# Optimization experiments

Hardware: AMD Instinct MI355X
Metric: run time of the kernel (lower is better)

The kernel has to match this reference:

```python
import jax, jax.numpy as jnp
import numpy as np

P, Q, R = 3, 1, 0          # CliffordAlgebra(p=3, q=1, r=0)
N = P + Q + R
ALG = 1 << N               # 16 basis blades
SHIFTS = (1, 2, 4)


def _cayley():
    """Cayley table C[i,j,k]: blade_i * blade_j = C[i,j,i^j] * blade_{i^j}."""
    metric = [1.0] * P + [-1.0] * Q + [0.0] * R
    C = np.zeros((ALG, ALG, ALG), np.float32)
    for a in range(ALG):
        for b in range(ALG):
            x = a >> 1
            s = 0
            while x:                       # reordering sign
                s += bin(x & b).count('1')
                x >>= 1
            val = -1.0 if (s & 1) else 1.0
            for i in range(N):             # metric for repeated basis vectors
                if (a & b) >> i & 1:
                    val *= metric[i]
            C[a, b, a ^ b] = val
    return C

_C = _cayley()
C0 = jnp.asarray(_C[:, :, 0])                        # grade-0 slice: <a*b>_0
A = jnp.asarray((_C - _C.transpose(1, 0, 2)) / 2.0)  # antisym: (ab - ba)/2
VEC_MASK = jnp.asarray(np.array([1.0 if bin(i).count('1') == 1 else 0.0 for i in range(ALG)], np.float32))
BIV_MASK = jnp.asarray(np.array([1.0 if bin(i).count('1') == 2 else 0.0 for i in range(ALG)], np.float32))


def setup_inputs() -> dict:
    key = jax.random.key(0)
    k1, k2 = jax.random.split(key, 2)
    B, T, D = 8, 4096, 1024
    return {
        "x": jax.random.normal(k1, (B, T, D), jnp.float32),
        "gate_w": jax.random.normal(k2, (D, 1), jnp.float32) * 0.02,
        "gate_b": jnp.zeros((1,), jnp.float32),
        "scalar_weight": jnp.float32(0.5),
        "bivector_weight": jnp.float32(0.5),
    }


def reference(x, gate_w, gate_b, scalar_weight, bivector_weight):
    B, T, D = x.shape
    n = D // ALG                         # 64 chunks of 16 (D divisible, no pad)
    ss = jax.nn.sigmoid(scalar_weight)
    sb = jax.nn.sigmoid(bivector_weight)
    gate = jax.nn.sigmoid(x @ gate_w + gate_b)   # (B,T,1), gate of x (loop-invariant)
    xc = x.reshape(B, T, n, ALG)
    out = x
    for shift in SHIFTS:                 # T=4096 > shift always
        c = x - jnp.roll(x, shift, axis=1)
        cc = c.reshape(B, T, n, ALG)
        # inner product: scalar part per chunk, summed over chunks
        scalar = jnp.einsum('btni,btnj,ij->bt', xc, cc, C0)
        # wedge: antisymmetrized geometric product of vector-grade projections
        av = xc * VEC_MASK
        bv = cc * VEC_MASK
        wedge = jnp.einsum('btni,btnj,ijk->btnk', av, bv, A) * BIV_MASK
        delta = (sb * wedge).reshape(B, T, D)
        delta = delta.at[..., 0].add(ss * scalar)   # scalar_part lives at index 0
        out = out + gate * delta
    return out
```

## Files before the change

kernel.cpp:

```cpp
#include <hip/hip_runtime.h>
#include <math.h>


constexpr int T_DIM = 4096;
constexpr int D_DIM = 1024;

constexpr int QB0 = 0x8000;
constexpr int QB1 = 0x8055;
constexpr int QB2 = 0x80AA;

template <int PAT>
__device__ __forceinline__ float swz(float v) {
    return __int_as_float(__builtin_amdgcn_ds_swizzle(__float_as_int(v), PAT));
}

__device__ __forceinline__ float sigmoidf(float z) {
    return 1.0f / (1.0f + __expf(-z));
}

__global__ __launch_bounds__(256, 4) void clifford_kernel(
    const float* __restrict__ x,
    const float* __restrict__ gate_w,
    const float* __restrict__ gate_b,
    const float* __restrict__ scalar_w,
    const float* __restrict__ bivec_w,
    float* __restrict__ out,
    int BT)
{
    int blk = blockIdx.x;
    if ((gridDim.x & 7) == 0) {
        const int per = gridDim.x >> 3;
        blk = (blockIdx.x & 7) * per + (blockIdx.x >> 3);
    }

    const int lane = threadIdx.x & 63;
    const int row  = blk * 4 + (threadIdx.x >> 6);
    if (row >= BT) return;
    const int b = row >> 12;
    const int t = row & (T_DIM - 1);
    const int sub = lane & 3;

    const float* __restrict__ r0 = x + (size_t)row * D_DIM;
    const size_t brow = (size_t)b * T_DIM;
    const float* __restrict__ r1 = x + (brow + ((t - 1) & (T_DIM - 1))) * D_DIM;
    const float* __restrict__ r2 = x + (brow + ((t - 2) & (T_DIM - 1))) * D_DIM;
    const float* __restrict__ r4 = x + (brow + ((t - 4) & (T_DIM - 1))) * D_DIM;

    float4 xv[4], q1[4], q2[4], q4[4], gv[4];
    #pragma unroll
    for (int m = 0; m < 4; ++m) {
        const int off = (lane << 2) + (m << 8);
        xv[m] = *(const float4*)(r0 + off);
        q1[m] = *(const float4*)(r1 + off);
        q2[m] = *(const float4*)(r2 + off);
        q4[m] = *(const float4*)(r4 + off);
        gv[m] = *(const float4*)(gate_w + off);
    }

    const float ss = sigmoidf(scalar_w[0]);
    const float sb = sigmoidf(bivec_w[0]);
    const float gb = gate_b[0];

    float4 ws;
    if      (sub == 0) ws = make_float4( 1.f,  1.f,  1.f, -1.f);
    else if (sub == 1) ws = make_float4( 1.f, -1.f, -1.f, -1.f);
    else if (sub == 2) ws = make_float4(-1.f,  1.f,  1.f,  1.f);
    else               ws = make_float4( 1.f,  1.f,  1.f, -1.f);
    const float m3  = (sub == 0) ? 1.f : 0.f;
    const float a1  = (sub == 1) ? 1.f : 0.f;
    const float a2  = (sub == 2) ? 1.f : 0.f;
    const float m12 = (sub == 3) ? 1.f : 0.f;

    float gate_part = 0.f, sc_part = 0.f;
    float4 dl[4];

    #pragma unroll
    for (int m = 0; m < 4; ++m) {
        float4 cs;
        cs.x = 3.f * xv[m].x - q1[m].x - q2[m].x - q4[m].x;
        cs.y = 3.f * xv[m].y - q1[m].y - q2[m].y - q4[m].y;
        cs.z = 3.f * xv[m].z - q1[m].z - q2[m].z - q4[m].z;
        cs.w = 3.f * xv[m].w - q1[m].w - q2[m].w - q4[m].w;

        gate_part += xv[m].x * gv[m].x + xv[m].y * gv[m].y
                   + xv[m].z * gv[m].z + xv[m].w * gv[m].w;
        sc_part   += ws.x * (xv[m].x * cs.x) + ws.y * (xv[m].y * cs.y)
                   + ws.z * (xv[m].z * cs.z) + ws.w * (xv[m].w * cs.w);

        const float x1  = swz<QB0>(xv[m].y), x2  = swz<QB0>(xv[m].z);
        const float x4b = swz<QB1>(xv[m].x), x8b = swz<QB2>(xv[m].x);
        const float c1  = swz<QB0>(cs.y),    c2  = swz<QB0>(cs.z);
        const float c4b = swz<QB1>(cs.x),    c8b = swz<QB2>(cs.x);

        const float w3  = x1 * c2  - x2  * c1;
        const float w5  = x1 * c4b - x4b * c1;
        const float w6  = x2 * c4b - x4b * c2;
        const float w9  = x1 * c8b - x8b * c1;
        const float w10 = x2 * c8b - x8b * c2;
        const float w12 = x4b * c8b - x8b * c4b;

        dl[m] = make_float4(m12 * w12,
                            a1 * w5 + a2 * w9,
                            a1 * w6 + a2 * w10,
                            m3 * w3);
    }

    #pragma unroll
    for (int o = 32; o > 0; o >>= 1) {
        gate_part += __shfl_xor(gate_part, o, 64);
        sc_part   += __shfl_xor(sc_part,   o, 64);
    }
    const float gate = sigmoidf(gate_part + gb);
    const float gsb  = gate * sb;

    float* __restrict__ orow = out + (size_t)row * D_DIM;
    #pragma unroll
    for (int m = 0; m < 4; ++m) {
        float4 o4;
        o4.x = xv[m].x + gsb * dl[m].x;
        o4.y = xv[m].y + gsb * dl[m].y;
        o4.z = xv[m].z + gsb * dl[m].z;
        o4.w = xv[m].w + gsb * dl[m].w;
        if (m == 0 && lane == 0) o4.x += gate * ss * sc_part;
        *(float4*)(orow + (lane << 2) + (m << 8)) = o4;
    }
}

extern "C" void kernel_launch(void* const* d_in, const int* in_sizes, int n_in,
                              void* d_out, int out_size, void* d_ws, size_t ws_size,
                              hipStream_t stream) {
    const float* x  = (const float*)d_in[0];
    const float* gw = (const float*)d_in[1];
    const float* gb = (const float*)d_in[2];
    const float* sw = (const float*)d_in[3];
    const float* bw = (const float*)d_in[4];
    float* out = (float*)d_out;

    const int BT = in_sizes[0] / D_DIM;
    const int blocks = (BT + 3) / 4;
    hipLaunchKernelGGL(clifford_kernel, dim3(blocks), dim3(256), 0, stream,
                       x, gw, gb, sw, bw, out, BT);
}
```

Measured before the change: 241.8 us.

## Process strips of 16 time rows per block with register ring buffer reuse

Each block now walks a strip of 16 consecutive time rows, keeping a ring of 8 row vectors in registers. The shifted rows (t-1, t-2, t-4) are reused from that ring instead of being reloaded per row, which cuts redundant global/L2 reads of x by about 4x. Each row is split across the 4 waves of a block, so the reductions need a shared-memory exchange and a __syncthreads per row. Loads run PF rows ahead to hide latency, and launch bounds are raised to 6 waves per SIMD. The per-row barrier and the smaller grid may limit parallelism.

```diff
diff --git a/kernel.cpp b/kernel.cpp
--- a/kernel.cpp
+++ b/kernel.cpp
@@ -2,8 +2,11 @@
 #include <math.h>
 
 
-constexpr int T_DIM = 4096;
-constexpr int D_DIM = 1024;
+constexpr int T_DIM   = 4096;
+constexpr int D_DIM   = 1024;
+constexpr int L_STRIP = 16;
+constexpr int PF      = 3;
+constexpr int WARM    = 4;
 
 constexpr int QB0 = 0x8000;
 constexpr int QB1 = 0x8055;
@@ -18,44 +21,44 @@
     return 1.0f / (1.0f + __expf(-z));
 }
 
-__global__ __launch_bounds__(256, 4) void clifford_kernel(
+__global__ __launch_bounds__(256, 6) void clifford_kernel(
     const float* __restrict__ x,
     const float* __restrict__ gate_w,
     const float* __restrict__ gate_b,
     const float* __restrict__ scalar_w,
     const float* __restrict__ bivec_w,
     float* __restrict__ out,
-    int BT)
+    int nstrips)
 {
     int blk = blockIdx.x;
     if ((gridDim.x & 7) == 0) {
         const int per = gridDim.x >> 3;
         blk = (blockIdx.x & 7) * per + (blockIdx.x >> 3);
     }
+    if (blk >= nstrips) return;
 
-    const int lane = threadIdx.x & 63;
-    const int row  = blk * 4 + (threadIdx.x >> 6);
-    if (row >= BT) return;
-    const int b = row >> 12;
-    const int t = row & (T_DIM - 1);
-    const int sub = lane & 3;
+    const int tid  = threadIdx.x;
+    const int wid  = tid >> 6;
+    const int lane = tid & 63;
+    const int sub  = tid & 3;
 
-    const float* __restrict__ r0 = x + (size_t)row * D_DIM;
-    const size_t brow = (size_t)b * T_DIM;
-    const float* __restrict__ r1 = x + (brow + ((t - 1) & (T_DIM - 1))) * D_DIM;
-    const float* __restrict__ r2 = x + (brow + ((t - 2) & (T_DIM - 1))) * D_DIM;
-    const float* __restrict__ r4 = x + (brow + ((t - 4) & (T_DIM - 1))) * D_DIM;
+    const int spb = T_DIM / L_STRIP;
+    const int b   = blk / spb;
+    const int t0  = (blk - b * spb) * L_STRIP;
 
-    float4 xv[4], q1[4], q2[4], q4[4], gv[4];
+    const int col = tid << 2;
+    const float* __restrict__ xb = x   + ((size_t)b * T_DIM) * D_DIM + col;
+    float*       __restrict__ ob = out + ((size_t)b * T_DIM + t0) * D_DIM + col;
+
+    __shared__ float red[2][4][2];
+
+    float4 s[8];
     #pragma unroll
-    for (int m = 0; m < 4; ++m) {
-        const int off = (lane << 2) + (m << 8);
-        xv[m] = *(const float4*)(r0 + off);
-        q1[m] = *(const float4*)(r1 + off);
-        q2[m] = *(const float4*)(r2 + off);
-        q4[m] = *(const float4*)(r4 + off);
-        gv[m] = *(const float4*)(gate_w + off);
+    for (int j = 0; j < WARM + PF; ++j) {
+        const int trow = (t0 - WARM + j) & (T_DIM - 1);
+        s[(j + 4) & 7] = *(const float4*)(xb + (size_t)trow * D_DIM);
     }
+    const float4 gv = *(const float4*)(gate_w + col);
 
     const float ss = sigmoidf(scalar_w[0]);
     const float sb = sigmoidf(bivec_w[0]);
@@ -71,26 +74,31 @@
     const float a2  = (sub == 2) ? 1.f : 0.f;
     const float m12 = (sub == 3) ? 1.f : 0.f;
 
-    float gate_part = 0.f, sc_part = 0.f;
-    float4 dl[4];
+    #pragma unroll
+    for (int k = 0; k < L_STRIP; ++k) {
+        if (k + PF < L_STRIP) {
+            s[(k + PF) & 7] = *(const float4*)(xb + (size_t)(t0 + k + PF) * D_DIM);
+        }
 
-    #pragma unroll
-    for (int m = 0; m < 4; ++m) {
+        const float4 cur = s[k & 7];
+        const float4 p1  = s[(k + 7) & 7];
+        const float4 p2  = s[(k + 6) & 7];
+        const float4 p4  = s[(k + 4) & 7];
+
         float4 cs;
-        cs.x = 3.f * xv[m].x - q1[m].x - q2[m].x - q4[m].x;
-        cs.y = 3.f * xv[m].y - q1[m].y - q2[m].y - q4[m].y;
-        cs.z = 3.f * xv[m].z - q1[m].z - q2[m].z - q4[m].z;
-        cs.w = 3.f * xv[m].w - q1[m].w - q2[m].w - q4[m].w;
+        cs.x = 3.f * cur.x - p1.x - p2.x - p4.x;
+        cs.y = 3.f * cur.y - p1.y - p2.y - p4.y;
+        cs.z = 3.f * cur.z - p1.z - p2.z - p4.z;
+        cs.w = 3.f * cur.w - p1.w - p2.w - p4.w;
 
-        gate_part += xv[m].x * gv[m].x + xv[m].y * gv[m].y
-                   + xv[m].z * gv[m].z + xv[m].w * gv[m].w;
-        sc_part   += ws.x * (xv[m].x * cs.x) + ws.y * (xv[m].y * cs.y)
-                   + ws.z * (xv[m].z * cs.z) + ws.w * (xv[m].w * cs.w);
+        float gp = cur.x * gv.x + cur.y * gv.y + cur.z * gv.z + cur.w * gv.w;
+        float sc = ws.x * (cur.x * cs.x) + ws.y * (cur.y * cs.y)
+                 + ws.z * (cur.z * cs.z) + ws.w * (cur.w * cs.w);
 
-        const float x1  = swz<QB0>(xv[m].y), x2  = swz<QB0>(xv[m].z);
-        const float x4b = swz<QB1>(xv[m].x), x8b = swz<QB2>(xv[m].x);
-        const float c1  = swz<QB0>(cs.y),    c2  = swz<QB0>(cs.z);
-        const float c4b = swz<QB1>(cs.x),    c8b = swz<QB2>(cs.x);
+        const float x1  = swz<QB0>(cur.y), x2  = swz<QB0>(cur.z);
+        const float x4b = swz<QB1>(cur.x), x8b = swz<QB2>(cur.x);
+        const float c1  = swz<QB0>(cs.y),  c2  = swz<QB0>(cs.z);
+        const float c4b = swz<QB1>(cs.x),  c8b = swz<QB2>(cs.x);
 
         const float w3  = x1 * c2  - x2  * c1;
         const float w5  = x1 * c4b - x4b * c1;
@@ -99,30 +107,37 @@
         const float w10 = x2 * c8b - x8b * c2;
         const float w12 = x4b * c8b - x8b * c4b;
 
-        dl[m] = make_float4(m12 * w12,
-                            a1 * w5 + a2 * w9,
-                            a1 * w6 + a2 * w10,
-                            m3 * w3);
-    }
+        const float4 dl = make_float4(m12 * w12,
+                                      a1 * w5 + a2 * w9,
+                                      a1 * w6 + a2 * w10,
+                                      m3 * w3);
 
-    #pragma unroll
-    for (int o = 32; o > 0; o >>= 1) {
-        gate_part += __shfl_xor(gate_part, o, 64);
-        sc_part   += __shfl_xor(sc_part,   o, 64);
-    }
-    const float gate = sigmoidf(gate_part + gb);
-    const float gsb  = gate * sb;
+        #pragma unroll
+        for (int o = 32; o > 0; o >>= 1) {
+            gp += __shfl_xor(gp, o, 64);
+            sc += __shfl_xor(sc, o, 64);
+        }
 
-    float* __restrict__ orow = out + (size_t)row * D_DIM;
-    #pragma unroll
-    for (int m = 0; m < 4; ++m) {
+        const int par = k & 1;
+        if (lane == 0) { red[par][wid][0] = gp; red[par][wid][1] = sc; }
+        __syncthreads();
+        float gsum = 0.f, scsum = 0.f;
+        #pragma unroll
+        for (int i = 0; i < 4; ++i) {
+            gsum  += red[par][i][0];
+            scsum += red[par][i][1];
+        }
+
+        const float gate = sigmoidf(gsum + gb);
+        const float gsb  = gate * sb;
+
         float4 o4;
-        o4.x = xv[m].x + gsb * dl[m].x;
-        o4.y = xv[m].y + gsb * dl[m].y;
-        o4.z = xv[m].z + gsb * dl[m].z;
-        o4.w = xv[m].w + gsb * dl[m].w;
-        if (m == 0 && lane == 0) o4.x += gate * ss * sc_part;
-        *(float4*)(orow + (lane << 2) + (m << 8)) = o4;
+        o4.x = cur.x + gsb * dl.x;
+        o4.y = cur.y + gsb * dl.y;
+        o4.z = cur.z + gsb * dl.z;
+        o4.w = cur.w + gsb * dl.w;
+        if (tid == 0) o4.x += gate * ss * scsum;
+        *(float4*)(ob + (size_t)k * D_DIM) = o4;
     }
 }
 
@@ -136,8 +151,8 @@
     const float* bw = (const float*)d_in[4];
     float* out = (float*)d_out;
 
-    const int BT = in_sizes[0] / D_DIM;
-    const int blocks = (BT + 3) / 4;
-    hipLaunchKernelGGL(clifford_kernel, dim3(blocks), dim3(256), 0, stream,
-                       x, gw, gb, sw, bw, out, BT);
+    const int BT      = in_sizes[0] / D_DIM;
+    const int nstrips = BT / L_STRIP;
+    hipLaunchKernelGGL(clifford_kernel, dim3(nstrips), dim3(256), 0, stream,
+                       x, gw, gb, sw, bw, out, nstrips);
 }
```

New measurement: 255.0 us. 1.05x slower.
